# Optimization experiments

Hardware: AMD Instinct MI355X
Metric: run time of the kernel (lower is better)

## Reference

```python
import jax, jax.numpy as jnp
import numpy as np

N = 262144       # rows
D = 256          # feature dim
CLUSTER = 512    # number of clusters


def setup_inputs() -> dict:
    key = jax.random.key(0)
    k1, k2 = jax.random.split(key)
    matrix = jax.random.normal(k1, (N, D), dtype=jnp.float32)
    label = jax.random.randint(k2, (N,), 0, CLUSTER, dtype=jnp.int32)
    return {"matrix": matrix, "label": label}


def reference(matrix, label):
    # Segment-mean: scatter-add rows into their cluster, divide by counts.
    # (Intended math of the original per-row loop + count-normalize.)
    sums = jax.ops.segment_sum(matrix, label, num_segments=CLUSTER)            # [C, D]
    counts = jax.ops.segment_sum(
        jnp.ones((matrix.shape[0],), matrix.dtype), label, num_segments=CLUSTER
    )                                                                          # [C]
    centers = sums / jnp.maximum(counts, 1.0)[:, None]                         # [C, D]

    # torch.nn.functional.pdist: L2 distance over all unordered pairs i<j.
    iu, ju = jnp.triu_indices(CLUSTER, k=1)                                    # static [P]
    diff = centers[iu] - centers[ju]                                           # [P, D]
    sq = jnp.sum(diff * diff, axis=-1)                                         # [P]
    dist = jnp.sqrt(jnp.maximum(sq, 1e-12))                                    # eps-guard for sqrt grad
    return -jnp.mean(dist)
```

## Files before the change

### kernel.cpp

```cpp
#include <hip/hip_runtime.h>

#define NROWS   262144
#define DIM     256
#define CLUSTER 512
#define NPAIR   (CLUSTER * (CLUSTER - 1) / 2)
#define G       16
#define CPG     32
#define R       64
#define CHUNK   (NROWS / R)
#define CAP     256
#define PAIR_BLOCKS 2044

__global__ __launch_bounds__(256) void k_gather(const float* __restrict__ matrix,
                                                const int* __restrict__ label,
                                                float* __restrict__ partial,
                                                int* __restrict__ countpart) {
    int g = blockIdx.x & (G - 1);
    int r = blockIdx.x >> 4;
    int t = threadIdx.x;
    int w = t >> 6, lane = t & 63;
    int chunkStart = r * CHUNK;

    __shared__ float sums[CPG][DIM];
    __shared__ unsigned short list[4][CAP];
    __shared__ int cur[4];
    __shared__ int cnt[CPG];

    {
        float4* s4 = (float4*)&sums[0][0];
        for (int i = t; i < CPG * DIM / 4; i += 256) s4[i] = make_float4(0.f, 0.f, 0.f, 0.f);
        if (t < 4) cur[t] = 0;
        if (t < CPG) cnt[t] = 0;
    }
    __syncthreads();

    for (int i = t; i < CHUNK; i += 256) {
        int lab = label[chunkStart + i];
        if ((lab >> 5) == g) {
            int cl = lab & (CPG - 1);
            int cls = cl & 3;
            int q = cl >> 2;
            atomicAdd(&cnt[cl], 1);
            int pos = atomicAdd(&cur[cls], 1);
            if (pos < CAP) list[cls][pos] = (unsigned short)(i | (q << 12));
        }
    }
    __syncthreads();

    int m = min(cur[w], CAP);
    #pragma unroll 2
    for (int k = 0; k < m; ++k) {
        int e = list[w][k];
        int lidx = e & 0xFFF;
        int cl = ((e >> 12) << 2) | w;
        const float4* row = (const float4*)(matrix + (size_t)(chunkStart + lidx) * DIM);
        float4 v = row[lane];
        float4* dst = (float4*)&sums[cl][lane * 4];
        float4 s = *dst;
        s.x += v.x; s.y += v.y; s.z += v.z; s.w += v.w;
        *dst = s;
    }
    __syncthreads();

    const float4* s4 = (const float4*)&sums[0][0];
    #pragma unroll
    for (int f = 0; f < 8; ++f) {
        int idx = f * 256 + t;
        int cl = idx >> 6;
        int d4 = idx & 63;
        int c = g * CPG + cl;
        ((float4*)(partial + ((size_t)c * R + r) * DIM))[d4] = s4[idx];
    }
    if (t < CPG) countpart[r * CLUSTER + g * CPG + t] = cnt[t];
}

__global__ __launch_bounds__(256) void k_center(const float* __restrict__ partial,
                                                const int* __restrict__ countpart,
                                                float* __restrict__ centers) {
    int c = blockIdx.x, d = threadIdx.x;
    __shared__ float invc;
    if (d == 0) {
        int s = 0;
        for (int r = 0; r < R; ++r) s += countpart[r * CLUSTER + c];
        invc = 1.0f / (float)max(s, 1);
    }
    float acc = 0.f;
    const float* p = partial + (size_t)c * R * DIM + d;
    #pragma unroll 8
    for (int r = 0; r < R; ++r) acc += p[r * DIM];
    __syncthreads();
    centers[c * DIM + d] = acc * invc;
}

__device__ __forceinline__ long long tri_off(long long i) {
    return i * (2 * CLUSTER - i - 1) / 2;
}

__global__ __launch_bounds__(256) void k_pairs(const float* __restrict__ centers,
                                               float* __restrict__ partials) {
    int wave = threadIdx.x >> 6;
    int lane = threadIdx.x & 63;
    long long base = ((long long)blockIdx.x * 4 + wave) * 16;

    double sq = sqrt((double)((2LL * CLUSTER - 1) * (2LL * CLUSTER - 1) - 8 * base));
    int i = (int)(((2 * CLUSTER - 1) - sq) * 0.5);
    if (i < 0) i = 0;
    while (tri_off(i + 1) <= base) ++i;
    while (tri_off(i) > base) --i;
    int j = (int)(base - tri_off(i)) + i + 1;

    float wsum = 0.f;
    #pragma unroll 4
    for (int q = 0; q < 16; ++q) {
        const float4* ci = (const float4*)(centers + (size_t)i * DIM);
        const float4* cj = (const float4*)(centers + (size_t)j * DIM);
        float4 a = ci[lane], b = cj[lane];
        float dx = a.x - b.x, dy = a.y - b.y, dz = a.z - b.z, dw = a.w - b.w;
        float local = dx * dx + dy * dy + dz * dz + dw * dw;
        #pragma unroll
        for (int o = 32; o; o >>= 1) local += __shfl_xor(local, o, 64);
        wsum += sqrtf(fmaxf(local, 1e-12f));
        if (++j == CLUSTER) { ++i; j = i + 1; }
    }

    __shared__ float bsum[4];
    if (lane == 0) bsum[wave] = wsum;
    __syncthreads();
    if (threadIdx.x == 0)
        partials[blockIdx.x] = bsum[0] + bsum[1] + bsum[2] + bsum[3];
}

__global__ __launch_bounds__(256) void k_final(const float* __restrict__ partials, int nb,
                                               float* __restrict__ out) {
    __shared__ float s[256];
    float acc = 0.f;
    for (int i = threadIdx.x; i < nb; i += 256) acc += partials[i];
    s[threadIdx.x] = acc;
    __syncthreads();
    for (int d = 128; d; d >>= 1) {
        if (threadIdx.x < d) s[threadIdx.x] += s[threadIdx.x + d];
        __syncthreads();
    }
    if (threadIdx.x == 0) out[0] = -s[0] / (float)NPAIR;
}

extern "C" void kernel_launch(void* const* d_in, const int* in_sizes, int n_in,
                              void* d_out, int out_size, void* d_ws, size_t ws_size,
                              hipStream_t stream) {
    const float* matrix = (const float*)d_in[0];
    const int* label = (const int*)d_in[1];
    float* out = (float*)d_out;

    float* partial   = (float*)d_ws;
    float* centers   = partial + (size_t)CLUSTER * R * DIM;
    float* ppart     = centers + (size_t)CLUSTER * DIM;
    int*   countpart = (int*)(ppart + 4096);

    k_gather<<<G * R, 256, 0, stream>>>(matrix, label, partial, countpart);
    k_center<<<CLUSTER, 256, 0, stream>>>(partial, countpart, centers);
    k_pairs<<<PAIR_BLOCKS, 256, 0, stream>>>(centers, ppart);
    k_final<<<1, 256, 0, stream>>>(ppart, PAIR_BLOCKS, out);
}
```

Baseline: 400.1 us.

## Rewrite gather, center reduction and pairwise kernels with register accumulation and tiling

The gather kernel now builds per-cluster index lists and accumulates rows in registers instead of read-modify-writing an LDS sums array, with vectorized label loads. The center kernel reduces counts with wave shuffles and partials with float4 loads split across waves. The pairwise distance kernel switches to 16x16 center tiles staged in LDS, computing each tile pair per block with a validity mask for the diagonal. This removes LDS traffic and redundant global reloads, but relies on a per-cluster list cap of 96 rows per chunk.

New measurement: 386.7 us. 3.4% less time.

```diff
diff --git a/kernel.cpp b/kernel.cpp
--- a/kernel.cpp
+++ b/kernel.cpp
@@ -8,8 +8,11 @@
 #define CPG     32
 #define R       64
 #define CHUNK   (NROWS / R)
-#define CAP     256
-#define PAIR_BLOCKS 2044
+#define CAP2    96
+
+#define T       16
+#define NT      (CLUSTER / T)
+#define TP      (NT * (NT + 1) / 2)
 
 __global__ __launch_bounds__(256) void k_gather(const float* __restrict__ matrix,
                                                 const int* __restrict__ label,
@@ -21,113 +24,120 @@
     int w = t >> 6, lane = t & 63;
     int chunkStart = r * CHUNK;
 
-    __shared__ float sums[CPG][DIM];
-    __shared__ unsigned short list[4][CAP];
-    __shared__ int cur[4];
+    __shared__ unsigned short list[CPG][CAP2];
     __shared__ int cnt[CPG];
 
-    {
-        float4* s4 = (float4*)&sums[0][0];
-        for (int i = t; i < CPG * DIM / 4; i += 256) s4[i] = make_float4(0.f, 0.f, 0.f, 0.f);
-        if (t < 4) cur[t] = 0;
-        if (t < CPG) cnt[t] = 0;
+    if (t < CPG) cnt[t] = 0;
+    __syncthreads();
+
+    const int4* lab4 = (const int4*)(label + chunkStart);
+    for (int ii = t; ii < CHUNK / 4; ii += 256) {
+        int4 L = lab4[ii];
+        int base = ii << 2;
+        int lab, cl, pos;
+        lab = L.x; if ((lab >> 5) == g) { cl = lab & 31; pos = atomicAdd(&cnt[cl], 1); if (pos < CAP2) list[cl][pos] = (unsigned short)(base + 0); }
+        lab = L.y; if ((lab >> 5) == g) { cl = lab & 31; pos = atomicAdd(&cnt[cl], 1); if (pos < CAP2) list[cl][pos] = (unsigned short)(base + 1); }
+        lab = L.z; if ((lab >> 5) == g) { cl = lab & 31; pos = atomicAdd(&cnt[cl], 1); if (pos < CAP2) list[cl][pos] = (unsigned short)(base + 2); }
+        lab = L.w; if ((lab >> 5) == g) { cl = lab & 31; pos = atomicAdd(&cnt[cl], 1); if (pos < CAP2) list[cl][pos] = (unsigned short)(base + 3); }
     }
     __syncthreads();
 
-    for (int i = t; i < CHUNK; i += 256) {
-        int lab = label[chunkStart + i];
-        if ((lab >> 5) == g) {
-            int cl = lab & (CPG - 1);
-            int cls = cl & 3;
-            int q = cl >> 2;
-            atomicAdd(&cnt[cl], 1);
-            int pos = atomicAdd(&cur[cls], 1);
-            if (pos < CAP) list[cls][pos] = (unsigned short)(i | (q << 12));
+    if (t < CPG) countpart[r * CLUSTER + (g << 5) + t] = cnt[t];
+
+    #pragma unroll
+    for (int q = 0; q < 8; ++q) {
+        int cl = (q << 2) | w;
+        int m = min(cnt[cl], CAP2);
+        float4 acc = make_float4(0.f, 0.f, 0.f, 0.f);
+        #pragma unroll 4
+        for (int k = 0; k < m; ++k) {
+            int i = list[cl][k];
+            float4 v = ((const float4*)(matrix + (size_t)(chunkStart + i) * DIM))[lane];
+            acc.x += v.x; acc.y += v.y; acc.z += v.z; acc.w += v.w;
         }
+        int c = (g << 5) | cl;
+        ((float4*)(partial + ((size_t)c * R + r) * DIM))[lane] = acc;
     }
-    __syncthreads();
-
-    int m = min(cur[w], CAP);
-    #pragma unroll 2
-    for (int k = 0; k < m; ++k) {
-        int e = list[w][k];
-        int lidx = e & 0xFFF;
-        int cl = ((e >> 12) << 2) | w;
-        const float4* row = (const float4*)(matrix + (size_t)(chunkStart + lidx) * DIM);
-        float4 v = row[lane];
-        float4* dst = (float4*)&sums[cl][lane * 4];
-        float4 s = *dst;
-        s.x += v.x; s.y += v.y; s.z += v.z; s.w += v.w;
-        *dst = s;
-    }
-    __syncthreads();
-
-    const float4* s4 = (const float4*)&sums[0][0];
-    #pragma unroll
-    for (int f = 0; f < 8; ++f) {
-        int idx = f * 256 + t;
-        int cl = idx >> 6;
-        int d4 = idx & 63;
-        int c = g * CPG + cl;
-        ((float4*)(partial + ((size_t)c * R + r) * DIM))[d4] = s4[idx];
-    }
-    if (t < CPG) countpart[r * CLUSTER + g * CPG + t] = cnt[t];
 }
 
 __global__ __launch_bounds__(256) void k_center(const float* __restrict__ partial,
                                                 const int* __restrict__ countpart,
                                                 float* __restrict__ centers) {
-    int c = blockIdx.x, d = threadIdx.x;
+    int c = blockIdx.x, t = threadIdx.x;
+    int lane = t & 63, w = t >> 6;
+
     __shared__ float invc;
-    if (d == 0) {
-        int s = 0;
-        for (int r = 0; r < R; ++r) s += countpart[r * CLUSTER + c];
-        invc = 1.0f / (float)max(s, 1);
+    __shared__ __align__(16) float4 red4[4][64];
+
+    if (w == 0) {
+        int s = countpart[lane * CLUSTER + c];
+        #pragma unroll
+        for (int o = 32; o; o >>= 1) s += __shfl_xor(s, o, 64);
+        if (lane == 0) invc = 1.0f / (float)max(s, 1);
     }
-    float acc = 0.f;
-    const float* p = partial + (size_t)c * R * DIM + d;
-    #pragma unroll 8
-    for (int r = 0; r < R; ++r) acc += p[r * DIM];
+
+    const float4* p4 = (const float4*)(partial + (size_t)c * R * DIM);
+    float4 acc = make_float4(0.f, 0.f, 0.f, 0.f);
+    #pragma unroll
+    for (int k = 0; k < 16; ++k) {
+        float4 v = p4[(size_t)(w * 16 + k) * 64 + lane];
+        acc.x += v.x; acc.y += v.y; acc.z += v.z; acc.w += v.w;
+    }
+    red4[w][lane] = acc;
     __syncthreads();
-    centers[c * DIM + d] = acc * invc;
-}
 
-__device__ __forceinline__ long long tri_off(long long i) {
-    return i * (2 * CLUSTER - i - 1) / 2;
+    if (w == 0) {
+        float4 s0 = red4[0][lane], s1 = red4[1][lane], s2 = red4[2][lane], s3 = red4[3][lane];
+        float iv = invc;
+        float4 o;
+        o.x = (s0.x + s1.x + s2.x + s3.x) * iv;
+        o.y = (s0.y + s1.y + s2.y + s3.y) * iv;
+        o.z = (s0.z + s1.z + s2.z + s3.z) * iv;
+        o.w = (s0.w + s1.w + s2.w + s3.w) * iv;
+        ((float4*)(centers + (size_t)c * DIM))[lane] = o;
+    }
 }
 
 __global__ __launch_bounds__(256) void k_pairs(const float* __restrict__ centers,
                                                float* __restrict__ partials) {
-    int wave = threadIdx.x >> 6;
-    int lane = threadIdx.x & 63;
-    long long base = ((long long)blockIdx.x * 4 + wave) * 16;
+    int bid = blockIdx.x;
+    int I = 0, rem = bid;
+    while (rem >= NT - I) { rem -= NT - I; ++I; }
+    int J = I + rem;
 
-    double sq = sqrt((double)((2LL * CLUSTER - 1) * (2LL * CLUSTER - 1) - 8 * base));
-    int i = (int)(((2 * CLUSTER - 1) - sq) * 0.5);
-    if (i < 0) i = 0;
-    while (tri_off(i + 1) <= base) ++i;
-    while (tri_off(i) > base) --i;
-    int j = (int)(base - tri_off(i)) + i + 1;
+    __shared__ __align__(16) float cI[T][DIM + 4];
+    __shared__ __align__(16) float cJ[T][DIM + 4];
+    __shared__ float bsum[4];
 
-    float wsum = 0.f;
-    #pragma unroll 4
-    for (int q = 0; q < 16; ++q) {
-        const float4* ci = (const float4*)(centers + (size_t)i * DIM);
-        const float4* cj = (const float4*)(centers + (size_t)j * DIM);
-        float4 a = ci[lane], b = cj[lane];
+    int t = threadIdx.x;
+    int lane = t & 63, w = t >> 6;
+
+    for (int idx = t; idx < T * 64; idx += 256) {
+        int rr = idx >> 6, d4 = idx & 63;
+        float4 a = ((const float4*)(centers + (size_t)(I * T + rr) * DIM))[d4];
+        *(float4*)&cI[rr][d4 * 4] = a;
+        float4 b = ((const float4*)(centers + (size_t)(J * T + rr) * DIM))[d4];
+        *(float4*)&cJ[rr][d4 * 4] = b;
+    }
+    __syncthreads();
+
+    int ti = t >> 4, tj = t & 15;
+    float acc = 0.f;
+    #pragma unroll 8
+    for (int d4 = 0; d4 < 64; ++d4) {
+        float4 a = *(const float4*)&cI[ti][d4 * 4];
+        float4 b = *(const float4*)&cJ[tj][d4 * 4];
         float dx = a.x - b.x, dy = a.y - b.y, dz = a.z - b.z, dw = a.w - b.w;
-        float local = dx * dx + dy * dy + dz * dz + dw * dw;
-        #pragma unroll
-        for (int o = 32; o; o >>= 1) local += __shfl_xor(local, o, 64);
-        wsum += sqrtf(fmaxf(local, 1e-12f));
-        if (++j == CLUSTER) { ++i; j = i + 1; }
+        acc += dx * dx + dy * dy + dz * dz + dw * dw;
     }
+    bool valid = (I < J) || (ti < tj);
+    float dist = valid ? sqrtf(fmaxf(acc, 1e-12f)) : 0.f;
 
-    __shared__ float bsum[4];
-    if (lane == 0) bsum[wave] = wsum;
+    #pragma unroll
+    for (int o = 32; o; o >>= 1) dist += __shfl_xor(dist, o, 64);
+    if (lane == 0) bsum[w] = dist;
     __syncthreads();
-    if (threadIdx.x == 0)
-        partials[blockIdx.x] = bsum[0] + bsum[1] + bsum[2] + bsum[3];
+    if (t == 0) partials[bid] = bsum[0] + bsum[1] + bsum[2] + bsum[3];
 }
 
 __global__ __launch_bounds__(256) void k_final(const float* __restrict__ partials, int nb,
@@ -158,6 +168,6 @@
 
     k_gather<<<G * R, 256, 0, stream>>>(matrix, label, partial, countpart);
     k_center<<<CLUSTER, 256, 0, stream>>>(partial, countpart, centers);
-    k_pairs<<<PAIR_BLOCKS, 256, 0, stream>>>(centers, ppart);
-    k_final<<<1, 256, 0, stream>>>(ppart, PAIR_BLOCKS, out);
+    k_pairs<<<TP, 256, 0, stream>>>(centers, ppart);
+    k_final<<<1, 256, 0, stream>>>(ppart, TP, out);
 }
```
